# Kernel tuning notes

Measured on AMD Instinct MI355X. Metric: run time of the kernel, lower is better.

Reference implementation:

```python
import jax, jax.numpy as jnp
import numpy as np

B, N, D, H = 2, 1536, 1024, 16
DH = D // H
SCALE = DH ** -0.5


def setup_inputs() -> dict:
    key = jax.random.key(0)
    ks = jax.random.split(key, 16)
    s = D ** -0.5
    x = jax.random.normal(ks[0], (B, N, D), dtype=jnp.float32)
    # causal prior: 0 on/below diagonal, -1e9 above
    causal = jnp.tril(jnp.ones((N, N), dtype=bool))
    attn_bias = jnp.where(causal, 0.0, -1e9).astype(jnp.float32)[None, None]
    mk = lambda k, shp: jax.random.normal(k, shp, dtype=jnp.float32) * s
    return {
        "x": x,
        "attn_bias": attn_bias,
        "Wq": mk(ks[1], (D, D)), "bq": jnp.zeros((D,), jnp.float32),
        "Wk": mk(ks[2], (D, D)), "bk": jnp.zeros((D,), jnp.float32),
        "Wv": mk(ks[3], (D, D)), "bv": jnp.zeros((D,), jnp.float32),
        "Wg1": mk(ks[4], (D, D)), "bg1": jnp.zeros((D,), jnp.float32),
        "Wg2": mk(ks[5], (D, 1)), "bg2": jnp.zeros((1,), jnp.float32),
        "Wo": mk(ks[6], (D, D)), "bo": jnp.zeros((D,), jnp.float32),
    }


def reference(x, attn_bias, Wq, bq, Wk, bk, Wv, bv, Wg1, bg1, Wg2, bg2, Wo, bo):
    b, n, d = x.shape
    # projections -> [B, H, N, DH]
    split = lambda t: t.reshape(b, n, H, DH).swapaxes(1, 2)
    Q = split(x @ Wq + bq)
    K = split(x @ Wk + bk)
    V = split(x @ Wv + bv)
    # scores [B, H, N, N]
    attn = jnp.einsum("bhnd,bhmd->bhnm", Q, K) * SCALE + attn_bias
    attn = jax.nn.softmax(attn, axis=-1)
    # per-(batch, head, query) entropy over key axis
    entropy = -(attn * jnp.log(attn + 1e-6)).sum(-1)  # [B, H, N]
    # gate MLP (torch nn.GELU default is exact erf)
    gate = jax.nn.sigmoid(jax.nn.gelu(x @ Wg1 + bg1, approximate=False) @ Wg2 + bg2)  # [B, N, 1]
    attn = attn * gate[:, None, :, :]  # broadcast over heads, keys
    out = jnp.einsum("bhnm,bhmd->bhnd", attn, V)
    out = out.swapaxes(1, 2).reshape(b, n, d) @ Wo + bo
    return out, entropy
```

## Files before the change

kernel.cpp:

```cpp
#include <hip/hip_runtime.h>
#include <hip/hip_bf16.h>
#include <math.h>

#define Bsz  2
#define Nseq 1536
#define Dmod 1024
#define NH   16
#define DHd  64
#define MTOT (Bsz*Nseq)
#define SCALE 0.125f
#define BK   32

typedef short  short8 __attribute__((ext_vector_type(8)));
typedef float  f32x4  __attribute__((ext_vector_type(4)));
typedef unsigned short u16x4 __attribute__((ext_vector_type(4)));
typedef unsigned short ushortT;

__device__ __forceinline__ float b2f(__hip_bfloat16 v) { return __bfloat162float(v); }
__device__ __forceinline__ unsigned short f2bf(float f) {
    union { float f; unsigned u; } a; a.f = f;
    unsigned r = a.u + 0x7fffu + ((a.u >> 16) & 1u);
    return (unsigned short)(r >> 16);
}

__device__ __forceinline__ void gl2lds16(const ushortT* g, ushortT* lds) {
    __builtin_amdgcn_global_load_lds(
        (const __attribute__((address_space(1))) unsigned int*)(g),
        (__attribute__((address_space(3))) unsigned int*)(lds),
        16, 0, 0);
}

__global__ __launch_bounds__(256)
void cvt_x_kernel(const float* __restrict__ x, ushortT* __restrict__ xb)
{
    size_t i = ((size_t)blockIdx.x * 256 + threadIdx.x) * 4;
    float4 v = *(const float4*)(x + i);
    u16x4 o = { f2bf(v.x), f2bf(v.y), f2bf(v.z), f2bf(v.w) };
    *(u16x4*)(xb + i) = o;
}

__global__ __launch_bounds__(256)
void wt_kernel(const float* W0, const float* W1, const float* W2,
               const float* W3, const float* W4,
               ushortT* T0, ushortT* T1, ushortT* T2, ushortT* T3, ushortT* T4)
{
    __shared__ float tile[64][65];
    const int z = blockIdx.z;
    const float* W = z == 0 ? W0 : z == 1 ? W1 : z == 2 ? W2 : z == 3 ? W3 : W4;
    ushortT*     T = z == 0 ? T0 : z == 1 ? T1 : z == 2 ? T2 : z == 3 ? T3 : T4;
    const int k0 = blockIdx.x * 64, n0 = blockIdx.y * 64;
    const int t = threadIdx.x;
    for (int i = t; i < 4096; i += 256) {
        int r = i >> 6, c = i & 63;
        tile[r][c] = W[(size_t)(k0 + r) * 1024 + n0 + c];
    }
    __syncthreads();
    for (int i = t; i < 4096; i += 256) {
        int rn = i >> 6, ck = i & 63;
        T[(size_t)(n0 + rn) * 1024 + k0 + ck] = f2bf(tile[ck][rn]);
    }
}

__device__ __forceinline__
void gemm_core(const ushortT* __restrict__ A, const ushortT* __restrict__ Bt,
               int m0, int n0, ushortT* AsU, ushortT* BsU, f32x4 (&acc)[4][4])
{
    const int t = threadIdx.x;
    const int l = t & 63, w = t >> 6;
    const int wm = (w >> 1) * 64, wn = (w & 1) * 64;
    const int lm = l & 15, q = l >> 4;

    const int r0 = t >> 2, c0 = (t & 3) * 8;
    const ushortT* Ag0 = A  + (size_t)(m0 + r0) * 1024 + c0;
    const ushortT* Ag1 = Ag0 + (size_t)64 * 1024;
    const ushortT* Bg0 = Bt + (size_t)(n0 + r0) * 1024 + c0;
    const ushortT* Bg1 = Bg0 + (size_t)64 * 1024;
    ushortT* La0 = AsU + t * 8;
    ushortT* La1 = AsU + 2048 + t * 8;
    ushortT* Lb0 = BsU + t * 8;
    ushortT* Lb1 = BsU + 2048 + t * 8;

    for (int k0 = 0; k0 < 1024; k0 += BK) {
        gl2lds16(Ag0 + k0, La0);
        gl2lds16(Ag1 + k0, La1);
        gl2lds16(Bg0 + k0, Lb0);
        gl2lds16(Bg1 + k0, Lb1);
        __syncthreads();
        short8 af[4], bf[4];
#pragma unroll
        for (int i = 0; i < 4; ++i) {
            af[i] = *(const short8*)&AsU[(wm + i * 16 + lm) * 32 + q * 8];
            bf[i] = *(const short8*)&BsU[(wn + i * 16 + lm) * 32 + q * 8];
        }
#pragma unroll
        for (int i = 0; i < 4; ++i)
#pragma unroll
            for (int j = 0; j < 4; ++j)
                acc[i][j] = __builtin_amdgcn_mfma_f32_16x16x32_bf16(af[i], bf[j], acc[i][j], 0, 0, 0);
        __syncthreads();
    }
}

__global__ __launch_bounds__(256)
void gemm_qkvg(const ushortT* __restrict__ xb,
               const ushortT* Wt0, const ushortT* Wt1, const ushortT* Wt2, const ushortT* Wt3,
               const float* bz0, const float* bz1, const float* bz2, const float* bz3,
               ushortT* O0, ushortT* O1, ushortT* O2, ushortT* O3)
{
    __shared__ ushortT AsU[128 * 32];
    __shared__ ushortT BsU[128 * 32];
    const int z = blockIdx.z;
    const ushortT* Wt  = z == 0 ? Wt0 : z == 1 ? Wt1 : z == 2 ? Wt2 : Wt3;
    const float*  bias = z == 0 ? bz0 : z == 1 ? bz1 : z == 2 ? bz2 : bz3;
    ushortT*      O    = z == 0 ? O0  : z == 1 ? O1  : z == 2 ? O2  : O3;
    const int m0 = blockIdx.y * 128, n0 = blockIdx.x * 128;

    f32x4 acc[4][4] = {};
    gemm_core(xb, Wt, m0, n0, AsU, BsU, acc);

    const int t = threadIdx.x, l = t & 63, w = t >> 6;
    const int wm = (w >> 1) * 64, wn = (w & 1) * 64;
    const int lm = l & 15, q = l >> 4;
#pragma unroll
    for (int i = 0; i < 4; ++i)
#pragma unroll
        for (int j = 0; j < 4; ++j) {
            int n = n0 + wn + j * 16 + lm;
            float bn = bias[n];
#pragma unroll
            for (int r = 0; r < 4; ++r) {
                int m = m0 + wm + i * 16 + q * 4 + r;
                float v = acc[i][j][r] + bn;
                if (z == 0) v *= SCALE;
                if (z == 3) v = 0.5f * v * (1.0f + erff(v * 0.70710678118654752f));
                if (z == 2) {
                    int b = m / Nseq, nn = m - b * Nseq;
                    int h = n >> 6, dd = n & 63;
                    O[(size_t)((b * 16 + h) * 64 + dd) * Nseq + nn] = f2bf(v);
                } else {
                    O[(size_t)m * 1024 + n] = f2bf(v);
                }
            }
        }
}

__global__ __launch_bounds__(256)
void gemm_out(const ushortT* __restrict__ AO, const ushortT* __restrict__ WtO,
              const float* __restrict__ bias, float* __restrict__ C)
{
    __shared__ ushortT AsU[128 * 32];
    __shared__ ushortT BsU[128 * 32];
    const int m0 = blockIdx.y * 128, n0 = blockIdx.x * 128;

    f32x4 acc[4][4] = {};
    gemm_core(AO, WtO, m0, n0, AsU, BsU, acc);

    const int t = threadIdx.x, l = t & 63, w = t >> 6;
    const int wm = (w >> 1) * 64, wn = (w & 1) * 64;
    const int lm = l & 15, q = l >> 4;
#pragma unroll
    for (int i = 0; i < 4; ++i)
#pragma unroll
        for (int j = 0; j < 4; ++j) {
            int n = n0 + wn + j * 16 + lm;
            float bn = bias[n];
#pragma unroll
            for (int r = 0; r < 4; ++r) {
                int m = m0 + wm + i * 16 + q * 4 + r;
                C[(size_t)m * 1024 + n] = acc[i][j][r] + bn;
            }
        }
}

__global__ __launch_bounds__(256)
void gate_kernel(const __hip_bfloat16* __restrict__ G1, const float* __restrict__ Wg2,
                 const float* __restrict__ bg2, float* __restrict__ gate)
{
    const int row = blockIdx.x;
    const int t   = threadIdx.x;
    float s = 0.f;
    for (int k = t; k < Dmod; k += 256)
        s += b2f(G1[(size_t)row * Dmod + k]) * Wg2[k];
#pragma unroll
    for (int off = 32; off > 0; off >>= 1) s += __shfl_down(s, off, 64);
    __shared__ float red[4];
    if ((t & 63) == 0) red[t >> 6] = s;
    __syncthreads();
    if (t == 0) {
        float tot = red[0] + red[1] + red[2] + red[3] + bg2[0];
        gate[row] = 1.f / (1.f + __expf(-tot));
    }
}

__global__ __launch_bounds__(64)
void attn_mfma(const ushortT* __restrict__ Q, const ushortT* __restrict__ K,
               const ushortT* __restrict__ Vt, const float* __restrict__ gate,
               ushortT* __restrict__ AO, float* __restrict__ ent)
{
    __shared__ ushortT Ps[16][72];

    const int l  = threadIdx.x;
    const int ln = l & 15, q4 = l >> 4;
    const int bh = blockIdx.x, b = bh >> 4, h = bh & 15;
    const int q16 = (int)gridDim.y - 1 - (int)blockIdx.y;
    const int wq = q16 * 16;
    const int kd = wq >> 6;
    const int sb = (wq >> 4) & 3;

    const ushortT* Qp = Q + (size_t)(b * Nseq + wq + ln) * Dmod + h * DHd + q4 * 8;
    short8 qf0 = *(const short8*)(Qp);
    short8 qf1 = *(const short8*)(Qp + 32);

    float l_lane[4] = {0.f, 0.f, 0.f, 0.f};
    float t_lane[4] = {0.f, 0.f, 0.f, 0.f};
    f32x4 oacc[4] = {};

    const ushortT* Kbase = K  + (size_t)(b * Nseq) * Dmod + h * DHd + q4 * 8;
    const ushortT* Vbase = Vt + ((size_t)(b * 16 + h) * 64) * Nseq + q4 * 8;

    for (int kt = 0; kt < kd; ++kt) {
        const int k0 = kt * 64;
        const ushortT* Kp = Kbase + (size_t)(k0 + ln) * Dmod;
        const ushortT* Vp = Vbase + (size_t)ln * Nseq + k0;

        short8 vf0[4], vf1[4];
#pragma unroll
        for (int nb = 0; nb < 4; ++nb) {
            vf0[nb] = *(const short8*)(Vp + (size_t)nb * 16 * Nseq);
            vf1[nb] = *(const short8*)(Vp + (size_t)nb * 16 * Nseq + 32);
        }
        f32x4 sacc[4];
#pragma unroll
        for (int nb = 0; nb < 4; ++nb) {
            short8 kf0 = *(const short8*)(Kp + (size_t)nb * 16 * Dmod);
            short8 kf1 = *(const short8*)(Kp + (size_t)nb * 16 * Dmod + 32);
            f32x4 a = {};
            a = __builtin_amdgcn_mfma_f32_16x16x32_bf16(qf0, kf0, a, 0, 0, 0);
            a = __builtin_amdgcn_mfma_f32_16x16x32_bf16(qf1, kf1, a, 0, 0, 0);
            sacc[nb] = a;
        }
#pragma unroll
        for (int nb = 0; nb < 4; ++nb)
#pragma unroll
            for (int r = 0; r < 4; ++r) {
                float sv = sacc[nb][r];
                float ev = __expf(sv);
                l_lane[r] += ev;
                t_lane[r] += ev * sv;
                Ps[q4 * 4 + r][nb * 16 + ln] = f2bf(ev);
            }
        short8 pf0 = *(const short8*)&Ps[ln][q4 * 8];
        short8 pf1 = *(const short8*)&Ps[ln][32 + q4 * 8];
#pragma unroll
        for (int nb = 0; nb < 4; ++nb) {
            oacc[nb] = __builtin_amdgcn_mfma_f32_16x16x32_bf16(pf0, vf0[nb], oacc[nb], 0, 0, 0);
            oacc[nb] = __builtin_amdgcn_mfma_f32_16x16x32_bf16(pf1, vf1[nb], oacc[nb], 0, 0, 0);
        }
    }

    {
        const int k0 = kd * 64;
        const ushortT* Kp = Kbase + (size_t)(k0 + ln) * Dmod;
        const ushortT* Vp = Vbase + (size_t)ln * Nseq + k0;

        short8 vf0[4], vf1[4];
#pragma unroll
        for (int nb = 0; nb < 4; ++nb) {
            vf0[nb] = *(const short8*)(Vp + (size_t)nb * 16 * Nseq);
            vf1[nb] = *(const short8*)(Vp + (size_t)nb * 16 * Nseq + 32);
        }
        f32x4 sacc[4];
#pragma unroll
        for (int nb = 0; nb < 4; ++nb) {
            if (nb <= sb) {
                short8 kf0 = *(const short8*)(Kp + (size_t)nb * 16 * Dmod);
                short8 kf1 = *(const short8*)(Kp + (size_t)nb * 16 * Dmod + 32);
                f32x4 a = {};
                a = __builtin_amdgcn_mfma_f32_16x16x32_bf16(qf0, kf0, a, 0, 0, 0);
                a = __builtin_amdgcn_mfma_f32_16x16x32_bf16(qf1, kf1, a, 0, 0, 0);
                sacc[nb] = a;
            }
        }
#pragma unroll
        for (int nb = 0; nb < 4; ++nb)
#pragma unroll
            for (int r = 0; r < 4; ++r) {
                float ev = 0.f;
                if (nb < sb) {
                    float sv = sacc[nb][r];
                    ev = __expf(sv);
                    l_lane[r] += ev; t_lane[r] += ev * sv;
                } else if (nb == sb) {
                    float sv = sacc[nb][r];
                    float e = __expf(sv);
                    ev = (ln <= q4 * 4 + r) ? e : 0.f;
                    l_lane[r] += ev; t_lane[r] += ev * sv * (ev != 0.f ? 1.f : 0.f);
                }
                Ps[q4 * 4 + r][nb * 16 + ln] = f2bf(ev);
            }
        short8 pf0 = *(const short8*)&Ps[ln][q4 * 8];
        short8 pf1 = *(const short8*)&Ps[ln][32 + q4 * 8];
#pragma unroll
        for (int nb = 0; nb < 4; ++nb) {
            oacc[nb] = __builtin_amdgcn_mfma_f32_16x16x32_bf16(pf0, vf0[nb], oacc[nb], 0, 0, 0);
            oacc[nb] = __builtin_amdgcn_mfma_f32_16x16x32_bf16(pf1, vf1[nb], oacc[nb], 0, 0, 0);
        }
    }

    float sc[4];
#pragma unroll
    for (int r = 0; r < 4; ++r) {
        float lv = l_lane[r], tv = t_lane[r];
#pragma unroll
        for (int msk = 1; msk < 16; msk <<= 1) {
            lv += __shfl_xor(lv, msk, 16);
            tv += __shfl_xor(tv, msk, 16);
        }
        int qg = wq + q4 * 4 + r;
        float inv = 1.f / lv;
        if (ln == 0)
            ent[((size_t)b * NH + h) * Nseq + qg] = logf(lv) - tv * inv;
        sc[r] = gate[b * Nseq + qg] * inv;
    }
#pragma unroll
    for (int nb = 0; nb < 4; ++nb)
#pragma unroll
        for (int r = 0; r < 4; ++r) {
            int qg = wq + q4 * 4 + r;
            AO[(size_t)(b * Nseq + qg) * Dmod + h * DHd + nb * 16 + ln] =
                f2bf(oacc[nb][r] * sc[r]);
        }
}

extern "C" void kernel_launch(void* const* d_in, const int* in_sizes, int n_in,
                              void* d_out, int out_size, void* d_ws, size_t ws_size,
                              hipStream_t stream)
{
    const float* x   = (const float*)d_in[0];
    const float* Wq  = (const float*)d_in[2];
    const float* bq  = (const float*)d_in[3];
    const float* Wk  = (const float*)d_in[4];
    const float* bk  = (const float*)d_in[5];
    const float* Wv  = (const float*)d_in[6];
    const float* bv  = (const float*)d_in[7];
    const float* Wg1 = (const float*)d_in[8];
    const float* bg1 = (const float*)d_in[9];
    const float* Wg2 = (const float*)d_in[10];
    const float* bg2 = (const float*)d_in[11];
    const float* Wo  = (const float*)d_in[12];
    const float* bo  = (const float*)d_in[13];

    const size_t NE = (size_t)MTOT * Dmod;
    ushortT* p   = (ushortT*)d_ws;
    ushortT* Qw  = p; p += NE;
    ushortT* Kw  = p; p += NE;
    ushortT* Vtw = p; p += NE;
    ushortT* G1  = p; p += NE;
    ushortT* AO  = p; p += NE;
    ushortT* xb  = p; p += NE;
    ushortT* WtQ = p; p += (size_t)1024 * 1024;
    ushortT* WtK = p; p += (size_t)1024 * 1024;
    ushortT* WtV = p; p += (size_t)1024 * 1024;
    ushortT* WtG = p; p += (size_t)1024 * 1024;
    ushortT* WtO = p; p += (size_t)1024 * 1024;
    float*  gate = (float*)p;

    float* out_f = (float*)d_out;
    float* ent_f = out_f + NE;

    cvt_x_kernel<<<dim3(MTOT * Dmod / 1024), 256, 0, stream>>>(x, xb);
    wt_kernel<<<dim3(16, 16, 5), 256, 0, stream>>>(Wq, Wk, Wv, Wg1, Wo,
                                                   WtQ, WtK, WtV, WtG, WtO);
    gemm_qkvg<<<dim3(8, 24, 4), 256, 0, stream>>>(xb, WtQ, WtK, WtV, WtG,
                                                  bq, bk, bv, bg1, Qw, Kw, Vtw, G1);
    gate_kernel<<<dim3(MTOT), 256, 0, stream>>>((const __hip_bfloat16*)G1, Wg2, bg2, gate);
    attn_mfma<<<dim3(Bsz * NH, Nseq / 16), 64, 0, stream>>>(Qw, Kw, Vtw, gate, AO, ent_f);
    gemm_out<<<dim3(8, 24), 256, 0, stream>>>(AO, WtO, bo, out_f);
}
```

Before: 262.5 us.

## Fuse gate MLP into GEMM epilogue, merge prep kernels, widen attention query tile

```diff
diff --git a/kernel.cpp b/kernel.cpp
--- a/kernel.cpp
+++ b/kernel.cpp
@@ -31,25 +31,29 @@
 }
 
 __global__ __launch_bounds__(256)
-void cvt_x_kernel(const float* __restrict__ x, ushortT* __restrict__ xb)
-{
-    size_t i = ((size_t)blockIdx.x * 256 + threadIdx.x) * 4;
-    float4 v = *(const float4*)(x + i);
-    u16x4 o = { f2bf(v.x), f2bf(v.y), f2bf(v.z), f2bf(v.w) };
-    *(u16x4*)(xb + i) = o;
-}
-
-__global__ __launch_bounds__(256)
-void wt_kernel(const float* W0, const float* W1, const float* W2,
-               const float* W3, const float* W4,
-               ushortT* T0, ushortT* T1, ushortT* T2, ushortT* T3, ushortT* T4)
-{
+void prep_kernel(const float* W0, const float* W1, const float* W2,
+                 const float* W3, const float* W4,
+                 ushortT* T0, ushortT* T1, ushortT* T2, ushortT* T3, ushortT* T4,
+                 const float* __restrict__ x, ushortT* __restrict__ xb,
+                 float* __restrict__ glogit)
+{
+    const int z = blockIdx.z;
+    const int t = threadIdx.x;
+    if (z == 5) {
+        const int bi = blockIdx.y * 16 + blockIdx.x;
+        const size_t NEl = (size_t)MTOT * Dmod;
+        for (size_t i = ((size_t)bi * 256 + t) * 4; i < NEl; i += (size_t)256 * 256 * 4) {
+            float4 v = *(const float4*)(x + i);
+            u16x4 o = { f2bf(v.x), f2bf(v.y), f2bf(v.z), f2bf(v.w) };
+            *(u16x4*)(xb + i) = o;
+        }
+        if (t < 12) glogit[bi * 12 + t] = 0.f;
+        return;
+    }
     __shared__ float tile[64][65];
-    const int z = blockIdx.z;
     const float* W = z == 0 ? W0 : z == 1 ? W1 : z == 2 ? W2 : z == 3 ? W3 : W4;
     ushortT*     T = z == 0 ? T0 : z == 1 ? T1 : z == 2 ? T2 : z == 3 ? T3 : T4;
     const int k0 = blockIdx.x * 64, n0 = blockIdx.y * 64;
-    const int t = threadIdx.x;
     for (int i = t; i < 4096; i += 256) {
         int r = i >> 6, c = i & 63;
         tile[r][c] = W[(size_t)(k0 + r) * 1024 + n0 + c];
@@ -105,14 +109,14 @@
 void gemm_qkvg(const ushortT* __restrict__ xb,
                const ushortT* Wt0, const ushortT* Wt1, const ushortT* Wt2, const ushortT* Wt3,
                const float* bz0, const float* bz1, const float* bz2, const float* bz3,
-               ushortT* O0, ushortT* O1, ushortT* O2, ushortT* O3)
+               const float* __restrict__ Wg2,
+               ushortT* O0, ushortT* O1, ushortT* O2, float* __restrict__ glogit)
 {
     __shared__ ushortT AsU[128 * 32];
     __shared__ ushortT BsU[128 * 32];
     const int z = blockIdx.z;
     const ushortT* Wt  = z == 0 ? Wt0 : z == 1 ? Wt1 : z == 2 ? Wt2 : Wt3;
     const float*  bias = z == 0 ? bz0 : z == 1 ? bz1 : z == 2 ? bz2 : bz3;
-    ushortT*      O    = z == 0 ? O0  : z == 1 ? O1  : z == 2 ? O2  : O3;
     const int m0 = blockIdx.y * 128, n0 = blockIdx.x * 128;
 
     f32x4 acc[4][4] = {};
@@ -121,6 +125,37 @@
     const int t = threadIdx.x, l = t & 63, w = t >> 6;
     const int wm = (w >> 1) * 64, wn = (w & 1) * 64;
     const int lm = l & 15, q = l >> 4;
+
+    if (z == 3) {
+        float part[4][4] = {};
+#pragma unroll
+        for (int i = 0; i < 4; ++i)
+#pragma unroll
+            for (int j = 0; j < 4; ++j) {
+                int n = n0 + wn + j * 16 + lm;
+                float bn = bias[n];
+                float w2 = Wg2[n];
+#pragma unroll
+                for (int r = 0; r < 4; ++r) {
+                    float v = acc[i][j][r] + bn;
+                    v = 0.5f * v * (1.0f + erff(v * 0.70710678118654752f));
+                    part[i][r] += v * w2;
+                }
+            }
+#pragma unroll
+        for (int i = 0; i < 4; ++i)
+#pragma unroll
+            for (int r = 0; r < 4; ++r) {
+                float p = part[i][r];
+#pragma unroll
+                for (int msk = 1; msk < 16; msk <<= 1) p += __shfl_xor(p, msk, 16);
+                if (lm == 0)
+                    atomicAdd(&glogit[m0 + wm + i * 16 + q * 4 + r], p);
+            }
+        return;
+    }
+
+    ushortT* O = z == 0 ? O0 : z == 1 ? O1 : O2;
 #pragma unroll
     for (int i = 0; i < 4; ++i)
 #pragma unroll
@@ -132,7 +167,6 @@
                 int m = m0 + wm + i * 16 + q * 4 + r;
                 float v = acc[i][j][r] + bn;
                 if (z == 0) v *= SCALE;
-                if (z == 3) v = 0.5f * v * (1.0f + erff(v * 0.70710678118654752f));
                 if (z == 2) {
                     int b = m / Nseq, nn = m - b * Nseq;
                     int h = n >> 6, dd = n & 63;
@@ -172,164 +206,182 @@
         }
 }
 
-__global__ __launch_bounds__(256)
-void gate_kernel(const __hip_bfloat16* __restrict__ G1, const float* __restrict__ Wg2,
-                 const float* __restrict__ bg2, float* __restrict__ gate)
-{
-    const int row = blockIdx.x;
-    const int t   = threadIdx.x;
-    float s = 0.f;
-    for (int k = t; k < Dmod; k += 256)
-        s += b2f(G1[(size_t)row * Dmod + k]) * Wg2[k];
-#pragma unroll
-    for (int off = 32; off > 0; off >>= 1) s += __shfl_down(s, off, 64);
-    __shared__ float red[4];
-    if ((t & 63) == 0) red[t >> 6] = s;
-    __syncthreads();
-    if (t == 0) {
-        float tot = red[0] + red[1] + red[2] + red[3] + bg2[0];
-        gate[row] = 1.f / (1.f + __expf(-tot));
-    }
-}
-
 __global__ __launch_bounds__(64)
 void attn_mfma(const ushortT* __restrict__ Q, const ushortT* __restrict__ K,
-               const ushortT* __restrict__ Vt, const float* __restrict__ gate,
-               ushortT* __restrict__ AO, float* __restrict__ ent)
-{
-    __shared__ ushortT Ps[16][72];
+               const ushortT* __restrict__ Vt, const float* __restrict__ glogit,
+               const float* __restrict__ bg2, ushortT* __restrict__ AO,
+               float* __restrict__ ent)
+{
+    __shared__ ushortT Ps[32][72];
 
     const int l  = threadIdx.x;
     const int ln = l & 15, q4 = l >> 4;
     const int bh = blockIdx.x, b = bh >> 4, h = bh & 15;
-    const int q16 = (int)gridDim.y - 1 - (int)blockIdx.y;
-    const int wq = q16 * 16;
+    const int q32 = (int)gridDim.y - 1 - (int)blockIdx.y;
+    const int wq = q32 * 32;
     const int kd = wq >> 6;
-    const int sb = (wq >> 4) & 3;
+    const int sbmax = ((wq >> 4) & 3) + 1;
 
     const ushortT* Qp = Q + (size_t)(b * Nseq + wq + ln) * Dmod + h * DHd + q4 * 8;
-    short8 qf0 = *(const short8*)(Qp);
-    short8 qf1 = *(const short8*)(Qp + 32);
-
-    float l_lane[4] = {0.f, 0.f, 0.f, 0.f};
-    float t_lane[4] = {0.f, 0.f, 0.f, 0.f};
-    f32x4 oacc[4] = {};
+    short8 qf[2][2];
+    qf[0][0] = *(const short8*)(Qp);
+    qf[0][1] = *(const short8*)(Qp + 32);
+    qf[1][0] = *(const short8*)(Qp + (size_t)16 * Dmod);
+    qf[1][1] = *(const short8*)(Qp + (size_t)16 * Dmod + 32);
+
+    float l_lane[2][4] = {}, t_lane[2][4] = {};
+    f32x4 oacc[2][4] = {};
 
     const ushortT* Kbase = K  + (size_t)(b * Nseq) * Dmod + h * DHd + q4 * 8;
     const ushortT* Vbase = Vt + ((size_t)(b * 16 + h) * 64) * Nseq + q4 * 8;
 
+    short8 kc[4][2];
+    {
+        const ushortT* Kp = Kbase + (size_t)ln * Dmod;
+#pragma unroll
+        for (int nb = 0; nb < 4; ++nb) {
+            kc[nb][0] = *(const short8*)(Kp + (size_t)nb * 16 * Dmod);
+            kc[nb][1] = *(const short8*)(Kp + (size_t)nb * 16 * Dmod + 32);
+        }
+    }
+
     for (int kt = 0; kt < kd; ++kt) {
         const int k0 = kt * 64;
-        const ushortT* Kp = Kbase + (size_t)(k0 + ln) * Dmod;
         const ushortT* Vp = Vbase + (size_t)ln * Nseq + k0;
-
-        short8 vf0[4], vf1[4];
+        short8 vf[4][2];
 #pragma unroll
         for (int nb = 0; nb < 4; ++nb) {
-            vf0[nb] = *(const short8*)(Vp + (size_t)nb * 16 * Nseq);
-            vf1[nb] = *(const short8*)(Vp + (size_t)nb * 16 * Nseq + 32);
-        }
-        f32x4 sacc[4];
-#pragma unroll
-        for (int nb = 0; nb < 4; ++nb) {
-            short8 kf0 = *(const short8*)(Kp + (size_t)nb * 16 * Dmod);
-            short8 kf1 = *(const short8*)(Kp + (size_t)nb * 16 * Dmod + 32);
-            f32x4 a = {};
-            a = __builtin_amdgcn_mfma_f32_16x16x32_bf16(qf0, kf0, a, 0, 0, 0);
-            a = __builtin_amdgcn_mfma_f32_16x16x32_bf16(qf1, kf1, a, 0, 0, 0);
-            sacc[nb] = a;
-        }
-#pragma unroll
-        for (int nb = 0; nb < 4; ++nb)
-#pragma unroll
-            for (int r = 0; r < 4; ++r) {
-                float sv = sacc[nb][r];
-                float ev = __expf(sv);
-                l_lane[r] += ev;
-                t_lane[r] += ev * sv;
-                Ps[q4 * 4 + r][nb * 16 + ln] = f2bf(ev);
-            }
-        short8 pf0 = *(const short8*)&Ps[ln][q4 * 8];
-        short8 pf1 = *(const short8*)&Ps[ln][32 + q4 * 8];
-#pragma unroll
-        for (int nb = 0; nb < 4; ++nb) {
-            oacc[nb] = __builtin_amdgcn_mfma_f32_16x16x32_bf16(pf0, vf0[nb], oacc[nb], 0, 0, 0);
-            oacc[nb] = __builtin_amdgcn_mfma_f32_16x16x32_bf16(pf1, vf1[nb], oacc[nb], 0, 0, 0);
-        }
+            vf[nb][0] = *(const short8*)(Vp + (size_t)nb * 16 * Nseq);
+            vf[nb][1] = *(const short8*)(Vp + (size_t)nb * 16 * Nseq + 32);
+        }
+        short8 kn[4][2];
+        {
+            const ushortT* Kp = Kbase + (size_t)(k0 + 64 + ln) * Dmod;
+#pragma unroll
+            for (int nb = 0; nb < 4; ++nb) {
+                kn[nb][0] = *(const short8*)(Kp + (size_t)nb * 16 * Dmod);
+                kn[nb][1] = *(const short8*)(Kp + (size_t)nb * 16 * Dmod + 32);
+            }
+        }
+        f32x4 sacc[2][4];
+#pragma unroll
+        for (int g = 0; g < 2; ++g)
+#pragma unroll
+            for (int nb = 0; nb < 4; ++nb) {
+                f32x4 a = {};
+                a = __builtin_amdgcn_mfma_f32_16x16x32_bf16(qf[g][0], kc[nb][0], a, 0, 0, 0);
+                a = __builtin_amdgcn_mfma_f32_16x16x32_bf16(qf[g][1], kc[nb][1], a, 0, 0, 0);
+                sacc[g][nb] = a;
+            }
+#pragma unroll
+        for (int g = 0; g < 2; ++g)
+#pragma unroll
+            for (int nb = 0; nb < 4; ++nb)
+#pragma unroll
+                for (int r = 0; r < 4; ++r) {
+                    float sv = sacc[g][nb][r];
+                    float ev = __expf(sv);
+                    l_lane[g][r] += ev;
+                    t_lane[g][r] += ev * sv;
+                    Ps[g * 16 + q4 * 4 + r][nb * 16 + ln] = f2bf(ev);
+                }
+        short8 pf[2][2];
+#pragma unroll
+        for (int g = 0; g < 2; ++g) {
+            pf[g][0] = *(const short8*)&Ps[g * 16 + ln][q4 * 8];
+            pf[g][1] = *(const short8*)&Ps[g * 16 + ln][32 + q4 * 8];
+        }
+#pragma unroll
+        for (int g = 0; g < 2; ++g)
+#pragma unroll
+            for (int nb = 0; nb < 4; ++nb) {
+                oacc[g][nb] = __builtin_amdgcn_mfma_f32_16x16x32_bf16(pf[g][0], vf[nb][0], oacc[g][nb], 0, 0, 0);
+                oacc[g][nb] = __builtin_amdgcn_mfma_f32_16x16x32_bf16(pf[g][1], vf[nb][1], oacc[g][nb], 0, 0, 0);
+            }
+#pragma unroll
+        for (int nb = 0; nb < 4; ++nb) { kc[nb][0] = kn[nb][0]; kc[nb][1] = kn[nb][1]; }
     }
 
     {
         const int k0 = kd * 64;
-        const ushortT* Kp = Kbase + (size_t)(k0 + ln) * Dmod;
         const ushortT* Vp = Vbase + (size_t)ln * Nseq + k0;
-
-        short8 vf0[4], vf1[4];
+        short8 vf[4][2];
 #pragma unroll
         for (int nb = 0; nb < 4; ++nb) {
-            vf0[nb] = *(const short8*)(Vp + (size_t)nb * 16 * Nseq);
-            vf1[nb] = *(const short8*)(Vp + (size_t)nb * 16 * Nseq + 32);
-        }
-        f32x4 sacc[4];
-#pragma unroll
-        for (int nb = 0; nb < 4; ++nb) {
-            if (nb <= sb) {
-                short8 kf0 = *(const short8*)(Kp + (size_t)nb * 16 * Dmod);
-                short8 kf1 = *(const short8*)(Kp + (size_t)nb * 16 * Dmod + 32);
-                f32x4 a = {};
-                a = __builtin_amdgcn_mfma_f32_16x16x32_bf16(qf0, kf0, a, 0, 0, 0);
-                a = __builtin_amdgcn_mfma_f32_16x16x32_bf16(qf1, kf1, a, 0, 0, 0);
-                sacc[nb] = a;
-            }
+            vf[nb][0] = *(const short8*)(Vp + (size_t)nb * 16 * Nseq);
+            vf[nb][1] = *(const short8*)(Vp + (size_t)nb * 16 * Nseq + 32);
+        }
+        f32x4 sacc[2][4];
+#pragma unroll
+        for (int g = 0; g < 2; ++g)
+#pragma unroll
+            for (int nb = 0; nb < 4; ++nb)
+                if (nb <= sbmax) {
+                    f32x4 a = {};
+                    a = __builtin_amdgcn_mfma_f32_16x16x32_bf16(qf[g][0], kc[nb][0], a, 0, 0, 0);
+                    a = __builtin_amdgcn_mfma_f32_16x16x32_bf16(qf[g][1], kc[nb][1], a, 0, 0, 0);
+                    sacc[g][nb] = a;
+                }
+#pragma unroll
+        for (int g = 0; g < 2; ++g)
+#pragma unroll
+            for (int nb = 0; nb < 4; ++nb)
+#pragma unroll
+                for (int r = 0; r < 4; ++r) {
+                    float ev = 0.f;
+                    if (nb <= sbmax) {
+                        int kg = k0 + nb * 16 + ln;
+                        int qg = wq + g * 16 + q4 * 4 + r;
+                        float sv = sacc[g][nb][r];
+                        ev = (kg <= qg) ? __expf(sv) : 0.f;
+                        l_lane[g][r] += ev;
+                        t_lane[g][r] += ev * sv;
+                    }
+                    Ps[g * 16 + q4 * 4 + r][nb * 16 + ln] = f2bf(ev);
+                }
+        short8 pf[2][2];
+#pragma unroll
+        for (int g = 0; g < 2; ++g) {
+            pf[g][0] = *(const short8*)&Ps[g * 16 + ln][q4 * 8];
+            pf[g][1] = *(const short8*)&Ps[g * 16 + ln][32 + q4 * 8];
+        }
+#pragma unroll
+        for (int g = 0; g < 2; ++g)
+#pragma unroll
+            for (int nb = 0; nb < 4; ++nb) {
+                oacc[g][nb] = __builtin_amdgcn_mfma_f32_16x16x32_bf16(pf[g][0], vf[nb][0], oacc[g][nb], 0, 0, 0);
+                oacc[g][nb] = __builtin_amdgcn_mfma_f32_16x16x32_bf16(pf[g][1], vf[nb][1], oacc[g][nb], 0, 0, 0);
+            }
+    }
+
+    const float bg2v = bg2[0];
+#pragma unroll
+    for (int g = 0; g < 2; ++g) {
+        float sc[4];
+#pragma unroll
+        for (int r = 0; r < 4; ++r) {
+            float lv = l_lane[g][r], tv = t_lane[g][r];
+#pragma unroll
+            for (int msk = 1; msk < 16; msk <<= 1) {
+                lv += __shfl_xor(lv, msk, 16);
+                tv += __shfl_xor(tv, msk, 16);
+            }
+            int qg = wq + g * 16 + q4 * 4 + r;
+            float inv = 1.f / lv;
+            if (ln == 0)
+                ent[((size_t)b * NH + h) * Nseq + qg] = logf(lv) - tv * inv;
+            float logit = glogit[b * Nseq + qg] + bg2v;
+            sc[r] = inv / (1.f + __expf(-logit));
         }
 #pragma unroll
         for (int nb = 0; nb < 4; ++nb)
 #pragma unroll
             for (int r = 0; r < 4; ++r) {
-                float ev = 0.f;
-                if (nb < sb) {
-                    float sv = sacc[nb][r];
-                    ev = __expf(sv);
-                    l_lane[r] += ev; t_lane[r] += ev * sv;
-                } else if (nb == sb) {
-                    float sv = sacc[nb][r];
-                    float e = __expf(sv);
-                    ev = (ln <= q4 * 4 + r) ? e : 0.f;
-                    l_lane[r] += ev; t_lane[r] += ev * sv * (ev != 0.f ? 1.f : 0.f);
-                }
-                Ps[q4 * 4 + r][nb * 16 + ln] = f2bf(ev);
-            }
-        short8 pf0 = *(const short8*)&Ps[ln][q4 * 8];
-        short8 pf1 = *(const short8*)&Ps[ln][32 + q4 * 8];
-#pragma unroll
-        for (int nb = 0; nb < 4; ++nb) {
-            oacc[nb] = __builtin_amdgcn_mfma_f32_16x16x32_bf16(pf0, vf0[nb], oacc[nb], 0, 0, 0);
-            oacc[nb] = __builtin_amdgcn_mfma_f32_16x16x32_bf16(pf1, vf1[nb], oacc[nb], 0, 0, 0);
-        }
-    }
-
-    float sc[4];
-#pragma unroll
-    for (int r = 0; r < 4; ++r) {
-        float lv = l_lane[r], tv = t_lane[r];
-#pragma unroll
-        for (int msk = 1; msk < 16; msk <<= 1) {
-            lv += __shfl_xor(lv, msk, 16);
-            tv += __shfl_xor(tv, msk, 16);
-        }
-        int qg = wq + q4 * 4 + r;
-        float inv = 1.f / lv;
-        if (ln == 0)
-            ent[((size_t)b * NH + h) * Nseq + qg] = logf(lv) - tv * inv;
-        sc[r] = gate[b * Nseq + qg] * inv;
-    }
-#pragma unroll
-    for (int nb = 0; nb < 4; ++nb)
-#pragma unroll
-        for (int r = 0; r < 4; ++r) {
-            int qg = wq + q4 * 4 + r;
-            AO[(size_t)(b * Nseq + qg) * Dmod + h * DHd + nb * 16 + ln] =
-                f2bf(oacc[nb][r] * sc[r]);
-        }
+                int qg = wq + g * 16 + q4 * 4 + r;
+                AO[(size_t)(b * Nseq + qg) * Dmod + h * DHd + nb * 16 + ln] =
+                    f2bf(oacc[g][nb][r] * sc[r]);
+            }
+    }
 }
 
 extern "C" void kernel_launch(void* const* d_in, const int* in_sizes, int n_in,
@@ -355,7 +407,6 @@
     ushortT* Qw  = p; p += NE;
     ushortT* Kw  = p; p += NE;
     ushortT* Vtw = p; p += NE;
-    ushortT* G1  = p; p += NE;
     ushortT* AO  = p; p += NE;
     ushortT* xb  = p; p += NE;
     ushortT* WtQ = p; p += (size_t)1024 * 1024;
@@ -363,17 +414,18 @@
     ushortT* WtV = p; p += (size_t)1024 * 1024;
     ushortT* WtG = p; p += (size_t)1024 * 1024;
     ushortT* WtO = p; p += (size_t)1024 * 1024;
-    float*  gate = (float*)p;
+    float* glogit = (float*)p;
 
     float* out_f = (float*)d_out;
     float* ent_f = out_f + NE;
 
-    cvt_x_kernel<<<dim3(MTOT * Dmod / 1024), 256, 0, stream>>>(x, xb);
-    wt_kernel<<<dim3(16, 16, 5), 256, 0, stream>>>(Wq, Wk, Wv, Wg1, Wo,
-                                                   WtQ, WtK, WtV, WtG, WtO);
+    prep_kernel<<<dim3(16, 16, 6), 256, 0, stream>>>(Wq, Wk, Wv, Wg1, Wo,
+                                                     WtQ, WtK, WtV, WtG, WtO,
+                                                     x, xb, glogit);
     gemm_qkvg<<<dim3(8, 24, 4), 256, 0, stream>>>(xb, WtQ, WtK, WtV, WtG,
-                                                  bq, bk, bv, bg1, Qw, Kw, Vtw, G1);
-    gate_kernel<<<dim3(MTOT), 256, 0, stream>>>((const __hip_bfloat16*)G1, Wg2, bg2, gate);
-    attn_mfma<<<dim3(Bsz * NH, Nseq / 16), 64, 0, stream>>>(Qw, Kw, Vtw, gate, AO, ent_f);
+                                                  bq, bk, bv, bg1, Wg2,
+                                                  Qw, Kw, Vtw, glogit);
+    attn_mfma<<<dim3(Bsz * NH, Nseq / 32), 64, 0, stream>>>(Qw, Kw, Vtw, glogit,
+                                                            bg2, AO, ent_f);
     gemm_out<<<dim3(8, 24), 256, 0, stream>>>(AO, WtO, bo, out_f);
 }
```

Result: no change. 263.7 us (+0.5%).
